# Optimization experiments

Measured on AMD Instinct MI355X. Metric: run time of the kernel, lower is better.

The kernel has to match this reference:

```python
import jax, jax.numpy as jnp
import numpy as np

SCALE = 10.0
KB = 1.0  # kernel_bandwidth

B, D, P, M, K = 128, 128, 4, 100000, 10


def _sqdist(a, b):
    # a: [..., N, D], b: [..., M, D] -> squared euclidean [..., N, M]
    a2 = jnp.sum(a * a, axis=-1)[..., :, None]
    b2 = jnp.sum(b * b, axis=-1)[..., None, :]
    ab = jnp.einsum('...nd,...md->...nm', a, b)
    return jnp.maximum(a2 + b2 - 2.0 * ab, 0.0)


def setup_inputs() -> dict:
    key = jax.random.key(0)
    k1, k2, k3, k4, k5, k6, k7 = jax.random.split(key, 7)
    return {
        'global_img_feat': jax.random.normal(k1, (B, D), jnp.float32),
        'global_text_feat': jax.random.normal(k2, (B, D), jnp.float32),
        'local_img_feats': jax.random.normal(k3, (P, B, D), jnp.float32),
        'centers': jax.random.normal(k4, (P, M, D), jnp.float32),
        'cross_indices': jax.random.randint(k5, (B, K), 0, M, jnp.int64),
        'position': jax.random.randint(k6, (B,), 0, M, jnp.int64),
        'memory_vid': jax.random.randint(k7, (M,), 0, 1000, jnp.int64),
    }


def reference(global_img_feat, global_text_feat, local_img_feats, centers,
              cross_indices, position, memory_vid):
    b = global_img_feat.shape[0]
    # ---- global MMD alignment (text branch detached) ----
    img = global_img_feat / jnp.linalg.norm(global_img_feat, axis=1, keepdims=True)
    txt_d = jax.lax.stop_gradient(global_text_feat)
    txt = txt_d / jnp.linalg.norm(txt_d, axis=1, keepdims=True)
    inv2kb2 = 1.0 / (2.0 * KB * KB)
    k_xx = jnp.exp(-_sqdist(img, img) * inv2kb2)
    k_yy = jnp.exp(-_sqdist(txt, txt) * inv2kb2)
    k_xy = jnp.exp(-_sqdist(img, txt) * inv2kb2)
    off = ~jnp.eye(b, dtype=bool)
    denom = b * (b - 1)
    mmd = (jnp.sum(jnp.where(off, k_xx, 0.0)) / denom
           + jnp.sum(jnp.where(off, k_yy, 0.0)) / denom
           - 2.0 * jnp.mean(k_xy))
    # ---- local part contrastive loss (vectorized over P parts) ----
    m = centers.shape[1]
    pos_feat = centers[:, cross_indices]                       # [P,B,K,D]
    f2 = jnp.sum(local_img_feats ** 2, axis=-1)                # [P,B]
    p2 = jnp.sum(pos_feat ** 2, axis=-1)                       # [P,B,K]
    fp = jnp.einsum('pbd,pbkd->pbk', local_img_feats, pos_feat)
    pos_dist = jnp.sqrt(jnp.maximum(f2[..., None] + p2 - 2.0 * fp, 0.0))  # [P,B,K]
    neg_dist = jnp.sqrt(_sqdist(local_img_feats, centers))     # [P,B,M]
    # negative mask over memory slots (int indices are constants)
    neg_mask = jnp.ones((m,), bool).at[cross_indices.reshape(-1)].set(False)
    neg_mask = neg_mask.at[position].set(False)
    x = jnp.log(jnp.sum(jnp.exp(-SCALE * pos_dist), axis=-1))  # [P,B]
    y = jnp.log(jnp.sum(jnp.exp(-SCALE * neg_dist) * neg_mask[None, None, :], axis=-1))
    l = jnp.sum(-x + y, axis=1) / local_img_feats.shape[1]     # [P]
    l = jnp.where(jnp.isnan(l), 0.0, l)
    local_loss = jnp.sum(l) / local_img_feats.shape[0]
    total = local_loss + 1.0 * mmd
    pos_vid = memory_vid[cross_indices]                        # [B,K]
    return total, local_loss, mmd, pos_vid
```

## Files before the change

kernel.cpp:

```cpp
#include <hip/hip_runtime.h>
#include <math.h>

#define B_ 128
#define D_ 128
#define P_ 4
#define M_ 100000
#define K_ 10
#define SCALE_ 10.0f
#define NEG_BLOCKS 512
#define MMD_BLOCKS 128
#define POS_BLOCKS 128
#define D2_CUT 120.0f

typedef short bf16x8 __attribute__((ext_vector_type(8)));
typedef float floatx4 __attribute__((ext_vector_type(4)));

__device__ inline unsigned pack_bf16_trunc(unsigned f0, unsigned f1) {
    return __builtin_amdgcn_perm(f1, f0, 0x07060302u);
}

template <int CTRL>
__device__ inline float dpp_add(float v) {
    int x = __builtin_amdgcn_update_dpp(0, __builtin_bit_cast(int, v), CTRL, 0xF, 0xF, true);
    return v + __builtin_bit_cast(float, x);
}
__device__ inline float row16Sum(float v) {
    v = dpp_add<0xB1>(v);
    v = dpp_add<0x4E>(v);
    v = dpp_add<0x141>(v);
    v = dpp_add<0x140>(v);
    return v;
}
__device__ inline float waveSum64(float v) {
    v = row16Sum(v);
    v += __shfl_xor(v, 16, 64);
    v += __shfl_xor(v, 32, 64);
    return v;
}
__device__ inline float waveReduceSumOld(float v) {
    #pragma unroll
    for (int off = 32; off > 0; off >>= 1) v += __shfl_xor(v, off, 64);
    return v;
}
__device__ inline float blockReduce128(float v, float* sh2) {
    v = waveSum64(v);
    int wid = threadIdx.x >> 6;
    if ((threadIdx.x & 63) == 0) sh2[wid] = v;
    __syncthreads();
    float r = sh2[0] + sh2[1];
    __syncthreads();
    return r;
}

__global__ __launch_bounds__(128) void k_prep(const float* __restrict__ img,
                                              const float* __restrict__ txt,
                                              const float* __restrict__ local,
                                              float* imgT, float* txtT,
                                              float* a2i, float* a2t,
                                              float* f2w, float* s_neg,
                                              bf16x8* __restrict__ Apk) {
    __shared__ float sh2[2];
    int bid = blockIdx.x, t = threadIdx.x;
    if (bid < 256) {
        int row = bid & 127, which = bid >> 7;
        if (bid < 4) s_neg[bid * 128 + t] = 0.f;
        const float* src = which ? txt : img;
        float* dstT = which ? txtT : imgT;
        float* a2 = which ? a2t : a2i;
        float v = src[row * D_ + t];
        float s = blockReduce128(v * v, sh2);
        float n = v / sqrtf(s);
        dstT[t * 128 + row] = n;
        float s2 = blockReduce128(n * n, sh2);
        if (t == 0) a2[row] = s2;
    } else if (bid < 768) {
        int r = bid - 256;
        float v = local[(size_t)r * D_ + t];
        float s = blockReduce128(v * v, sh2);
        if (t == 0) f2w[r] = s;
    } else {
        int g = (bid - 768) * 128 + t;
        int p = g >> 11, f = g & 2047;
        int fl = f & 63, bt = (f >> 6) & 7, kc = f >> 9;
        int row = bt * 16 + (fl & 15);
        int col = kc * 32 + ((fl >> 4) & 3) * 8;
        const float* lp = local + (size_t)p * B_ * D_ + row * D_ + col;
        const uint4 u0 = *(const uint4*)lp;
        const uint4 u1 = *(const uint4*)(lp + 4);
        union { bf16x8 v; unsigned u[4]; } fr;
        fr.u[0] = pack_bf16_trunc(u0.x, u0.y);
        fr.u[1] = pack_bf16_trunc(u0.z, u0.w);
        fr.u[2] = pack_bf16_trunc(u1.x, u1.y);
        fr.u[3] = pack_bf16_trunc(u1.z, u1.w);
        Apk[g] = fr.v;
    }
}

__global__ __launch_bounds__(256, 2) void k_neg(const float* __restrict__ centers,
                                                const int* __restrict__ ci,
                                                const int* __restrict__ posi,
                                                const float* __restrict__ f2w,
                                                const bf16x8* __restrict__ Apk,
                                                float* __restrict__ s_neg) {
    __shared__ float Bt[2][3][2048];
    const int t = threadIdx.x;
    const int w = t >> 6;
    const int l = t & 63;
    const int bid = blockIdx.x;
    const int p = bid >> 7;
    const int g = bid & 127;
    const int pp = w >> 1;
    const int hm = w & 1;
    const int pairid = 2 * g + pp;
    const int nt = (g < 53) ? 25 : 24;
    const int n16 = l & 15;
    const int q = l >> 4;

    const bf16x8* Ap = Apk + (p << 11);
    bf16x8 af[4][4];
    #pragma unroll
    for (int kc = 0; kc < 4; kc++)
        #pragma unroll
        for (int b4 = 0; b4 < 4; b4++)
            af[kc][b4] = Ap[kc * 512 + (hm * 4 + b4) * 64 + l];
    floatx4 f2r[4];
    #pragma unroll
    for (int b4 = 0; b4 < 4; b4++)
        f2r[b4] = *(const floatx4*)&f2w[p * 128 + (hm * 4 + b4) * 16 + q * 4];

    unsigned srcoff[4];
    #pragma unroll
    for (int j = 0; j < 4; j++) {
        unsigned x = (unsigned)(hm * 4096 + j * 1024 + l * 16);
        unsigned s = (x >> 9) & 7u;
        srcoff[j] = x ^ (s << 4);
    }

    const char* tb0 = (const char*)(centers + (size_t)p * M_ * D_);
    char* myBt = (char*)&Bt[pp][0][0];

    auto DMA = [&](int tl, int buf) {
        const char* src = tb0 + (size_t)tl * 8192;
        char* dst = myBt + buf * 8192 + hm * 4096;
        #pragma unroll
        for (int j = 0; j < 4; j++) {
            __builtin_amdgcn_global_load_lds(
                (const __attribute__((address_space(1))) void*)(src + srcoff[j]),
                (__attribute__((address_space(3))) void*)(dst + j * 1024),
                16, 0, 0);
        }
    };

    float sacc[4][4];
    #pragma unroll
    for (int b4 = 0; b4 < 4; b4++)
        #pragma unroll
        for (int r = 0; r < 4; r++) sacc[b4][r] = 0.f;

    DMA(pairid, 0);
    if (nt > 1) DMA(pairid + 256, 1);
    asm volatile("s_waitcnt vmcnt(4)" ::: "memory");
    __builtin_amdgcn_s_barrier();

    int tli = pairid;
    int ib = 0;
    const unsigned sw = (unsigned)((n16 & 7) << 4);
    for (int i = 0; i < nt; i++) {
        const char* bb = myBt + ib * 8192;
        float c2 = 0.f;
        bf16x8 bfr[4];
        #pragma unroll
        for (int kc = 0; kc < 4; kc++) {
            unsigned t0a = (unsigned)(n16 * 512 + kc * 128 + q * 32);
            union { floatx4 f; uint4 u; } h0, h1;
            h0.f = *(const floatx4*)(bb + (t0a ^ sw));
            h1.f = *(const floatx4*)(bb + ((t0a + 16) ^ sw));
            c2 += h0.f[0]*h0.f[0] + h0.f[1]*h0.f[1] + h0.f[2]*h0.f[2] + h0.f[3]*h0.f[3]
                + h1.f[0]*h1.f[0] + h1.f[1]*h1.f[1] + h1.f[2]*h1.f[2] + h1.f[3]*h1.f[3];
            union { bf16x8 v; unsigned uu[4]; } fr;
            fr.uu[0] = pack_bf16_trunc(h0.u.x, h0.u.y);
            fr.uu[1] = pack_bf16_trunc(h0.u.z, h0.u.w);
            fr.uu[2] = pack_bf16_trunc(h1.u.x, h1.u.y);
            fr.uu[3] = pack_bf16_trunc(h1.u.z, h1.u.w);
            bfr[kc] = fr.v;
        }
        c2 += __shfl_xor(c2, 16, 64);
        c2 += __shfl_xor(c2, 32, 64);
        const float c2v = c2;

        floatx4 acc[4];
        #pragma unroll
        for (int b4 = 0; b4 < 4; b4++) acc[b4] = (floatx4)(0.f);
        #pragma unroll
        for (int kc = 0; kc < 4; kc++) {
            #pragma unroll
            for (int b4 = 0; b4 < 4; b4++)
                acc[b4] = __builtin_amdgcn_mfma_f32_16x16x32_bf16(af[kc][b4], bfr[kc], acc[b4], 0, 0, 0);
        }

        float dmin = 1e30f;
        #pragma unroll
        for (int b4 = 0; b4 < 4; b4++) {
            #pragma unroll
            for (int r = 0; r < 4; r++) {
                float d2 = fmaf(-2.f, acc[b4][r], f2r[b4][r] + c2v);
                dmin = fminf(dmin, d2);
            }
        }
        if (__any(dmin < D2_CUT)) {
            const int gm = tli * 16 + n16;
            float vm = 1.f;
            for (int ii = 0; ii < B_ * K_; ii++) {
                if (ci[ii] == gm) vm = 0.f;
            }
            for (int ii = 0; ii < B_; ii++) {
                if (posi[ii] == gm) vm = 0.f;
            }
            #pragma unroll
            for (int b4 = 0; b4 < 4; b4++) {
                #pragma unroll
                for (int r = 0; r < 4; r++) {
                    float d2 = fmaxf(fmaf(-2.f, acc[b4][r], f2r[b4][r] + c2v), 0.f);
                    if (d2 < D2_CUT) sacc[b4][r] += vm * expf(-SCALE_ * sqrtf(d2));
                }
            }
        }

        if (i + 2 < nt) {
            int b2 = ib + 2; if (b2 >= 3) b2 -= 3;
            DMA(tli + 512, b2);
            asm volatile("s_waitcnt vmcnt(4)" ::: "memory");
        } else if (i + 1 < nt) {
            asm volatile("s_waitcnt vmcnt(0)" ::: "memory");
        }
        __builtin_amdgcn_s_barrier();

        tli += 256;
        ib = (ib + 1 == 3) ? 0 : ib + 1;
    }

    #pragma unroll
    for (int b4 = 0; b4 < 4; b4++) {
        #pragma unroll
        for (int r = 0; r < 4; r++) {
            float s = row16Sum(sacc[b4][r]);
            if (n16 == 0 && s != 0.f)
                atomicAdd(&s_neg[p * 128 + (hm * 4 + b4) * 16 + q * 4 + r], s);
        }
    }
}

__global__ __launch_bounds__(256) void k_mp(const float* __restrict__ local,
                                            const float* __restrict__ centers,
                                            const float* __restrict__ imgT,
                                            const float* __restrict__ txtT,
                                            const float* __restrict__ a2i,
                                            const float* __restrict__ a2t,
                                            const int* __restrict__ ci,
                                            const int* __restrict__ mvid,
                                            const float* __restrict__ f2w,
                                            float* __restrict__ s_pos,
                                            double* __restrict__ mmd_part,
                                            float* __restrict__ out) {
    __shared__ float ri[128], rt[128], sh2[2];
    const int bid = blockIdx.x;
    const int t = threadIdx.x;
    const int w = t >> 6;
    const int l = t & 63;

    if (bid < MMD_BLOCKS) {
        const int i = bid;
        if (t < 128) {
            ri[t] = imgT[t * 128 + i];
            rt[t] = txtT[t * 128 + i];
        }
        __syncthreads();
        float kxx = 0.f, kyy = 0.f, kxy = 0.f;
        if (t < 128) {
            float dxx = 0.f, dyy = 0.f, dxy = 0.f;
            #pragma unroll 4
            for (int d = 0; d < D_; d++) {
                float rid = ri[d], rtd = rt[d];
                float av = imgT[d * 128 + t];
                float bv = txtT[d * 128 + t];
                dxx = fmaf(rid, av, dxx);
                dyy = fmaf(rtd, bv, dyy);
                dxy = fmaf(rid, bv, dxy);
            }
            kxx = (i == t) ? 0.f : expf(-fmaxf(a2i[i] + a2i[t] - 2.f * dxx, 0.f) * 0.5f);
            kyy = (i == t) ? 0.f : expf(-fmaxf(a2t[i] + a2t[t] - 2.f * dyy, 0.f) * 0.5f);
            kxy = expf(-fmaxf(a2i[i] + a2t[t] - 2.f * dxy, 0.f) * 0.5f);
        }
        float sxx = waveReduceSumOld(kxx);
        float syy = waveReduceSumOld(kyy);
        float sxy = waveReduceSumOld(kxy);
        __syncthreads();
        if (t == 0)  { sh2[0] = sxx; }
        if (t == 64) { sh2[1] = sxx; }
        __syncthreads();
        float txx = sh2[0] + sh2[1];
        __syncthreads();
        if (t == 0)  { sh2[0] = syy; }
        if (t == 64) { sh2[1] = syy; }
        __syncthreads();
        float tyy = sh2[0] + sh2[1];
        __syncthreads();
        if (t == 0)  { sh2[0] = sxy; }
        if (t == 64) { sh2[1] = sxy; }
        __syncthreads();
        float txy = sh2[0] + sh2[1];
        if (t == 0) {
            mmd_part[i] = (double)txx;
            mmd_part[128 + i] = (double)tyy;
            mmd_part[256 + i] = (double)txy;
        }
    } else {
        const int pair = (bid - MMD_BLOCKS) * 4 + w;
        const int p = pair >> 7, b = pair & 127;
        const float* f = local + (size_t)pair * D_;
        float f0 = f[l], f1 = f[l + 64];
        float f2v = f2w[pair];
        const float* cb = centers + (size_t)p * M_ * D_;
        float s = 0.f;
        #pragma unroll
        for (int k = 0; k < K_; k++) {
            int idx = ci[b * K_ + k];
            const float* c = cb + (size_t)idx * D_;
            float c0 = c[l], c1 = c[l + 64];
            float p2 = waveSum64(c0 * c0 + c1 * c1);
            float fp = waveSum64(f0 * c0 + f1 * c1);
            float d2 = fmaxf(f2v + p2 - 2.f * fp, 0.f);
            if (d2 < D2_CUT) s += expf(-SCALE_ * sqrtf(d2));
        }
        if (l == 0) s_pos[pair] = s;
        if (p == 0 && l < K_) {
            int ix = ci[b * K_ + l];
            out[3 + b * K_ + l] = (float)mvid[ix];
        }
    }
}

__global__ __launch_bounds__(512) void k_final(const float* __restrict__ s_pos,
                                               const float* __restrict__ s_neg,
                                               const double* __restrict__ mmd_part,
                                               float* out) {
    __shared__ float red[512];
    __shared__ float lp_[4];
    int t = threadIdx.x;
    float x = logf(s_pos[t]);
    float y = logf(s_neg[t]);
    red[t] = -x + y;
    __syncthreads();
    for (int s = 64; s > 0; s >>= 1) {
        if ((t & 127) < s) red[t] += red[t + s];
        __syncthreads();
    }
    if ((t & 127) == 0) {
        float lv = red[t] / (float)B_;
        if (isnan(lv)) lv = 0.f;
        lp_[t >> 7] = lv;
    }
    __syncthreads();
    if (t == 0) {
        float local_loss = (lp_[0] + lp_[1] + lp_[2] + lp_[3]) / (float)P_;
        double sxx = 0.0, syy = 0.0, sxy = 0.0;
        for (int i = 0; i < 128; i++) {
            sxx += mmd_part[i];
            syy += mmd_part[128 + i];
            sxy += mmd_part[256 + i];
        }
        double denom = 128.0 * 127.0;
        float mmd = (float)(sxx / denom + syy / denom - 2.0 * (sxy / (128.0 * 128.0)));
        out[0] = local_loss + mmd;
        out[1] = local_loss;
        out[2] = mmd;
    }
}

extern "C" void kernel_launch(void* const* d_in, const int* in_sizes, int n_in,
                              void* d_out, int out_size, void* d_ws, size_t ws_size,
                              hipStream_t stream) {
    const float* img     = (const float*)d_in[0];
    const float* txt     = (const float*)d_in[1];
    const float* local   = (const float*)d_in[2];
    const float* centers = (const float*)d_in[3];
    const int*   ci      = (const int*)d_in[4];
    const int*   posi    = (const int*)d_in[5];
    const int*   mvid    = (const int*)d_in[6];
    float* out = (float*)d_out;

    char* ws = (char*)d_ws;
    float*  imgT     = (float*)(ws + 0);
    float*  txtT     = (float*)(ws + 65536);
    float*  a2i      = (float*)(ws + 131072);
    float*  a2t      = (float*)(ws + 131584);
    float*  f2w      = (float*)(ws + 132096);
    float*  s_pos    = (float*)(ws + 134144);
    float*  s_neg    = (float*)(ws + 136192);
    double* mmd_part = (double*)(ws + 138240);
    bf16x8* Apk      = (bf16x8*)(ws + 147456);

    k_prep<<<832, 128, 0, stream>>>(img, txt, local, imgT, txtT, a2i, a2t, f2w, s_neg, Apk);
    k_neg<<<NEG_BLOCKS, 256, 0, stream>>>(centers, ci, posi, f2w, Apk, s_neg);
    k_mp<<<MMD_BLOCKS + POS_BLOCKS, 256, 0, stream>>>(
        local, centers, imgT, txtT, a2i, a2t, ci, mvid, f2w, s_pos, mmd_part, out);
    k_final<<<1, 512, 0, stream>>>(s_pos, s_neg, mmd_part, out);
}
```

Measured before the change: 324.2 us.

## Fuse neg and MMD/pos kernels; give each wave full 128-row tiles with private double buffer

Merges the negative-distance kernel and the MMD/positive kernel into one launch, so the small MMD and positive blocks can run alongside the large centers scan instead of after it. Each wave now covers all 128 batch rows against its own 16-center tile, which doubles the A fragments and accumulators held in registers. Each wave also keeps a private LDS double buffer, which removes the block-wide barrier and leaves only per-wave vmcnt waits. The cost is higher register pressure under launch_bounds(256,2), which may cause spills or lower occupancy.

```diff
diff --git a/kernel.cpp b/kernel.cpp
--- a/kernel.cpp
+++ b/kernel.cpp
@@ -96,183 +96,166 @@
     }
 }
 
-__global__ __launch_bounds__(256, 2) void k_neg(const float* __restrict__ centers,
-                                                const int* __restrict__ ci,
-                                                const int* __restrict__ posi,
-                                                const float* __restrict__ f2w,
-                                                const bf16x8* __restrict__ Apk,
-                                                float* __restrict__ s_neg) {
-    __shared__ float Bt[2][3][2048];
-    const int t = threadIdx.x;
-    const int w = t >> 6;
-    const int l = t & 63;
-    const int bid = blockIdx.x;
-    const int p = bid >> 7;
-    const int g = bid & 127;
-    const int pp = w >> 1;
-    const int hm = w & 1;
-    const int pairid = 2 * g + pp;
-    const int nt = (g < 53) ? 25 : 24;
-    const int n16 = l & 15;
-    const int q = l >> 4;
-
-    const bf16x8* Ap = Apk + (p << 11);
-    bf16x8 af[4][4];
-    #pragma unroll
-    for (int kc = 0; kc < 4; kc++)
-        #pragma unroll
-        for (int b4 = 0; b4 < 4; b4++)
-            af[kc][b4] = Ap[kc * 512 + (hm * 4 + b4) * 64 + l];
-    floatx4 f2r[4];
-    #pragma unroll
-    for (int b4 = 0; b4 < 4; b4++)
-        f2r[b4] = *(const floatx4*)&f2w[p * 128 + (hm * 4 + b4) * 16 + q * 4];
-
-    unsigned srcoff[4];
-    #pragma unroll
-    for (int j = 0; j < 4; j++) {
-        unsigned x = (unsigned)(hm * 4096 + j * 1024 + l * 16);
-        unsigned s = (x >> 9) & 7u;
-        srcoff[j] = x ^ (s << 4);
-    }
-
-    const char* tb0 = (const char*)(centers + (size_t)p * M_ * D_);
-    char* myBt = (char*)&Bt[pp][0][0];
-
-    auto DMA = [&](int tl, int buf) {
-        const char* src = tb0 + (size_t)tl * 8192;
-        char* dst = myBt + buf * 8192 + hm * 4096;
-        #pragma unroll
-        for (int j = 0; j < 4; j++) {
-            __builtin_amdgcn_global_load_lds(
-                (const __attribute__((address_space(1))) void*)(src + srcoff[j]),
-                (__attribute__((address_space(3))) void*)(dst + j * 1024),
-                16, 0, 0);
-        }
+__global__ __launch_bounds__(256, 2) void k_negmp(const float* __restrict__ centers,
+                                                  const float* __restrict__ local,
+                                                  const float* __restrict__ imgT,
+                                                  const float* __restrict__ txtT,
+                                                  const float* __restrict__ a2i,
+                                                  const float* __restrict__ a2t,
+                                                  const int* __restrict__ ci,
+                                                  const int* __restrict__ posi,
+                                                  const int* __restrict__ mvid,
+                                                  const float* __restrict__ f2w,
+                                                  const bf16x8* __restrict__ Apk,
+                                                  float* __restrict__ s_neg,
+                                                  float* __restrict__ s_pos,
+                                                  double* __restrict__ mmd_part,
+                                                  float* __restrict__ out) {
+    union Smem {
+        float Bt[4][2][2048];
+        struct { float ri[128], rt[128], sh2[2]; } m;
     };
-
-    float sacc[4][4];
-    #pragma unroll
-    for (int b4 = 0; b4 < 4; b4++)
-        #pragma unroll
-        for (int r = 0; r < 4; r++) sacc[b4][r] = 0.f;
-
-    DMA(pairid, 0);
-    if (nt > 1) DMA(pairid + 256, 1);
-    asm volatile("s_waitcnt vmcnt(4)" ::: "memory");
-    __builtin_amdgcn_s_barrier();
-
-    int tli = pairid;
-    int ib = 0;
-    const unsigned sw = (unsigned)((n16 & 7) << 4);
-    for (int i = 0; i < nt; i++) {
-        const char* bb = myBt + ib * 8192;
-        float c2 = 0.f;
-        bf16x8 bfr[4];
-        #pragma unroll
-        for (int kc = 0; kc < 4; kc++) {
-            unsigned t0a = (unsigned)(n16 * 512 + kc * 128 + q * 32);
-            union { floatx4 f; uint4 u; } h0, h1;
-            h0.f = *(const floatx4*)(bb + (t0a ^ sw));
-            h1.f = *(const floatx4*)(bb + ((t0a + 16) ^ sw));
-            c2 += h0.f[0]*h0.f[0] + h0.f[1]*h0.f[1] + h0.f[2]*h0.f[2] + h0.f[3]*h0.f[3]
-                + h1.f[0]*h1.f[0] + h1.f[1]*h1.f[1] + h1.f[2]*h1.f[2] + h1.f[3]*h1.f[3];
-            union { bf16x8 v; unsigned uu[4]; } fr;
-            fr.uu[0] = pack_bf16_trunc(h0.u.x, h0.u.y);
-            fr.uu[1] = pack_bf16_trunc(h0.u.z, h0.u.w);
-            fr.uu[2] = pack_bf16_trunc(h1.u.x, h1.u.y);
-            fr.uu[3] = pack_bf16_trunc(h1.u.z, h1.u.w);
-            bfr[kc] = fr.v;
-        }
-        c2 += __shfl_xor(c2, 16, 64);
-        c2 += __shfl_xor(c2, 32, 64);
-        const float c2v = c2;
-
-        floatx4 acc[4];
-        #pragma unroll
-        for (int b4 = 0; b4 < 4; b4++) acc[b4] = (floatx4)(0.f);
-        #pragma unroll
-        for (int kc = 0; kc < 4; kc++) {
-            #pragma unroll
-            for (int b4 = 0; b4 < 4; b4++)
-                acc[b4] = __builtin_amdgcn_mfma_f32_16x16x32_bf16(af[kc][b4], bfr[kc], acc[b4], 0, 0, 0);
-        }
-
-        float dmin = 1e30f;
-        #pragma unroll
-        for (int b4 = 0; b4 < 4; b4++) {
-            #pragma unroll
-            for (int r = 0; r < 4; r++) {
-                float d2 = fmaf(-2.f, acc[b4][r], f2r[b4][r] + c2v);
-                dmin = fminf(dmin, d2);
-            }
-        }
-        if (__any(dmin < D2_CUT)) {
-            const int gm = tli * 16 + n16;
-            float vm = 1.f;
-            for (int ii = 0; ii < B_ * K_; ii++) {
-                if (ci[ii] == gm) vm = 0.f;
-            }
-            for (int ii = 0; ii < B_; ii++) {
-                if (posi[ii] == gm) vm = 0.f;
-            }
-            #pragma unroll
-            for (int b4 = 0; b4 < 4; b4++) {
-                #pragma unroll
-                for (int r = 0; r < 4; r++) {
-                    float d2 = fmaxf(fmaf(-2.f, acc[b4][r], f2r[b4][r] + c2v), 0.f);
-                    if (d2 < D2_CUT) sacc[b4][r] += vm * expf(-SCALE_ * sqrtf(d2));
-                }
-            }
-        }
-
-        if (i + 2 < nt) {
-            int b2 = ib + 2; if (b2 >= 3) b2 -= 3;
-            DMA(tli + 512, b2);
-            asm volatile("s_waitcnt vmcnt(4)" ::: "memory");
-        } else if (i + 1 < nt) {
-            asm volatile("s_waitcnt vmcnt(0)" ::: "memory");
-        }
-        __builtin_amdgcn_s_barrier();
-
-        tli += 256;
-        ib = (ib + 1 == 3) ? 0 : ib + 1;
-    }
-
-    #pragma unroll
-    for (int b4 = 0; b4 < 4; b4++) {
-        #pragma unroll
-        for (int r = 0; r < 4; r++) {
-            float s = row16Sum(sacc[b4][r]);
-            if (n16 == 0 && s != 0.f)
-                atomicAdd(&s_neg[p * 128 + (hm * 4 + b4) * 16 + q * 4 + r], s);
-        }
-    }
-}
-
-__global__ __launch_bounds__(256) void k_mp(const float* __restrict__ local,
-                                            const float* __restrict__ centers,
-                                            const float* __restrict__ imgT,
-                                            const float* __restrict__ txtT,
-                                            const float* __restrict__ a2i,
-                                            const float* __restrict__ a2t,
-                                            const int* __restrict__ ci,
-                                            const int* __restrict__ mvid,
-                                            const float* __restrict__ f2w,
-                                            float* __restrict__ s_pos,
-                                            double* __restrict__ mmd_part,
-                                            float* __restrict__ out) {
-    __shared__ float ri[128], rt[128], sh2[2];
+    __shared__ Smem sm;
     const int bid = blockIdx.x;
     const int t = threadIdx.x;
     const int w = t >> 6;
     const int l = t & 63;
 
-    if (bid < MMD_BLOCKS) {
-        const int i = bid;
+    if (bid < NEG_BLOCKS) {
+        const int p = bid >> 7;
+        const int v = ((bid & 127) << 2) + w;
+        const int nt = (v < 106) ? 13 : 12;
+        const int n16 = l & 15;
+        const int q = l >> 4;
+
+        const bf16x8* Ap = Apk + (p << 11);
+        bf16x8 af[4][8];
+        #pragma unroll
+        for (int kc = 0; kc < 4; kc++)
+            #pragma unroll
+            for (int bt = 0; bt < 8; bt++)
+                af[kc][bt] = Ap[kc * 512 + bt * 64 + l];
+        floatx4 f2r[8];
+        #pragma unroll
+        for (int bt = 0; bt < 8; bt++)
+            f2r[bt] = *(const floatx4*)&f2w[p * 128 + bt * 16 + q * 4];
+
+        unsigned srcoff[8];
+        #pragma unroll
+        for (int j = 0; j < 8; j++) {
+            unsigned x = (unsigned)(j * 1024 + l * 16);
+            unsigned s = (x >> 9) & 7u;
+            srcoff[j] = x ^ (s << 4);
+        }
+
+        const char* tb0 = (const char*)(centers + (size_t)p * M_ * D_);
+        char* myBt = (char*)&sm.Bt[w][0][0];
+
+        auto DMA = [&](int tl, int buf) {
+            const char* src = tb0 + (size_t)tl * 8192;
+            char* dst = myBt + buf * 8192;
+            #pragma unroll
+            for (int j = 0; j < 8; j++) {
+                __builtin_amdgcn_global_load_lds(
+                    (const __attribute__((address_space(1))) void*)(src + srcoff[j]),
+                    (__attribute__((address_space(3))) void*)(dst + j * 1024),
+                    16, 0, 0);
+            }
+        };
+
+        float sacc[8][4];
+        #pragma unroll
+        for (int bt = 0; bt < 8; bt++)
+            #pragma unroll
+            for (int r = 0; r < 4; r++) sacc[bt][r] = 0.f;
+
+        DMA(v, 0);
+        DMA(v + 512, 1);
+
+        int tl = v;
+        const unsigned sw = (unsigned)((n16 & 7) << 4);
+        for (int i = 0; i < nt; i++) {
+            if (i + 1 < nt) asm volatile("s_waitcnt vmcnt(8)" ::: "memory");
+            else            asm volatile("s_waitcnt vmcnt(0)" ::: "memory");
+
+            const char* bb = myBt + (i & 1) * 8192;
+            float c2 = 0.f;
+            bf16x8 bfr[4];
+            #pragma unroll
+            for (int kc = 0; kc < 4; kc++) {
+                unsigned t0a = (unsigned)(n16 * 512 + kc * 128 + q * 32);
+                union { floatx4 f; uint4 u; } h0, h1;
+                h0.f = *(const floatx4*)(bb + (t0a ^ sw));
+                h1.f = *(const floatx4*)(bb + ((t0a + 16) ^ sw));
+                c2 += h0.f[0]*h0.f[0] + h0.f[1]*h0.f[1] + h0.f[2]*h0.f[2] + h0.f[3]*h0.f[3]
+                    + h1.f[0]*h1.f[0] + h1.f[1]*h1.f[1] + h1.f[2]*h1.f[2] + h1.f[3]*h1.f[3];
+                union { bf16x8 vv; unsigned uu[4]; } fr;
+                fr.uu[0] = pack_bf16_trunc(h0.u.x, h0.u.y);
+                fr.uu[1] = pack_bf16_trunc(h0.u.z, h0.u.w);
+                fr.uu[2] = pack_bf16_trunc(h1.u.x, h1.u.y);
+                fr.uu[3] = pack_bf16_trunc(h1.u.z, h1.u.w);
+                bfr[kc] = fr.vv;
+            }
+            c2 += __shfl_xor(c2, 16, 64);
+            c2 += __shfl_xor(c2, 32, 64);
+            const float c2v = c2;
+
+            floatx4 acc[8];
+            #pragma unroll
+            for (int bt = 0; bt < 8; bt++) acc[bt] = (floatx4)(0.f);
+            #pragma unroll
+            for (int kc = 0; kc < 4; kc++) {
+                #pragma unroll
+                for (int bt = 0; bt < 8; bt++)
+                    acc[bt] = __builtin_amdgcn_mfma_f32_16x16x32_bf16(af[kc][bt], bfr[kc], acc[bt], 0, 0, 0);
+            }
+
+            float dmin = 1e30f;
+            #pragma unroll
+            for (int bt = 0; bt < 8; bt++) {
+                #pragma unroll
+                for (int r = 0; r < 4; r++) {
+                    float d2 = fmaf(-2.f, acc[bt][r], f2r[bt][r] + c2v);
+                    dmin = fminf(dmin, d2);
+                }
+            }
+            if (__any(dmin < D2_CUT)) {
+                const int gm = tl * 16 + n16;
+                float vm = 1.f;
+                for (int ii = 0; ii < B_ * K_; ii++) {
+                    if (ci[ii] == gm) vm = 0.f;
+                }
+                for (int ii = 0; ii < B_; ii++) {
+                    if (posi[ii] == gm) vm = 0.f;
+                }
+                #pragma unroll
+                for (int bt = 0; bt < 8; bt++) {
+                    #pragma unroll
+                    for (int r = 0; r < 4; r++) {
+                        float d2 = fmaxf(fmaf(-2.f, acc[bt][r], f2r[bt][r] + c2v), 0.f);
+                        if (d2 < D2_CUT) sacc[bt][r] += vm * expf(-SCALE_ * sqrtf(d2));
+                    }
+                }
+            }
+
+            if (i + 2 < nt) DMA(tl + 1024, i & 1);
+            tl += 512;
+        }
+
+        #pragma unroll
+        for (int bt = 0; bt < 8; bt++) {
+            #pragma unroll
+            for (int r = 0; r < 4; r++) {
+                float s = row16Sum(sacc[bt][r]);
+                if (n16 == 0 && s != 0.f)
+                    atomicAdd(&s_neg[p * 128 + bt * 16 + q * 4 + r], s);
+            }
+        }
+    } else if (bid < NEG_BLOCKS + MMD_BLOCKS) {
+        const int i = bid - NEG_BLOCKS;
         if (t < 128) {
-            ri[t] = imgT[t * 128 + i];
-            rt[t] = txtT[t * 128 + i];
+            sm.m.ri[t] = imgT[t * 128 + i];
+            sm.m.rt[t] = txtT[t * 128 + i];
         }
         __syncthreads();
         float kxx = 0.f, kyy = 0.f, kxy = 0.f;
@@ -280,7 +263,7 @@
             float dxx = 0.f, dyy = 0.f, dxy = 0.f;
             #pragma unroll 4
             for (int d = 0; d < D_; d++) {
-                float rid = ri[d], rtd = rt[d];
+                float rid = sm.m.ri[d], rtd = sm.m.rt[d];
                 float av = imgT[d * 128 + t];
                 float bv = txtT[d * 128 + t];
                 dxx = fmaf(rid, av, dxx);
@@ -295,27 +278,27 @@
         float syy = waveReduceSumOld(kyy);
         float sxy = waveReduceSumOld(kxy);
         __syncthreads();
-        if (t == 0)  { sh2[0] = sxx; }
-        if (t == 64) { sh2[1] = sxx; }
-        __syncthreads();
-        float txx = sh2[0] + sh2[1];
-        __syncthreads();
-        if (t == 0)  { sh2[0] = syy; }
-        if (t == 64) { sh2[1] = syy; }
-        __syncthreads();
-        float tyy = sh2[0] + sh2[1];
-        __syncthreads();
-        if (t == 0)  { sh2[0] = sxy; }
-        if (t == 64) { sh2[1] = sxy; }
-        __syncthreads();
-        float txy = sh2[0] + sh2[1];
+        if (t == 0)  { sm.m.sh2[0] = sxx; }
+        if (t == 64) { sm.m.sh2[1] = sxx; }
+        __syncthreads();
+        float txx = sm.m.sh2[0] + sm.m.sh2[1];
+        __syncthreads();
+        if (t == 0)  { sm.m.sh2[0] = syy; }
+        if (t == 64) { sm.m.sh2[1] = syy; }
+        __syncthreads();
+        float tyy = sm.m.sh2[0] + sm.m.sh2[1];
+        __syncthreads();
+        if (t == 0)  { sm.m.sh2[0] = sxy; }
+        if (t == 64) { sm.m.sh2[1] = sxy; }
+        __syncthreads();
+        float txy = sm.m.sh2[0] + sm.m.sh2[1];
         if (t == 0) {
             mmd_part[i] = (double)txx;
             mmd_part[128 + i] = (double)tyy;
             mmd_part[256 + i] = (double)txy;
         }
     } else {
-        const int pair = (bid - MMD_BLOCKS) * 4 + w;
+        const int pair = (bid - (NEG_BLOCKS + MMD_BLOCKS)) * 4 + w;
         const int p = pair >> 7, b = pair & 127;
         const float* f = local + (size_t)pair * D_;
         float f0 = f[l], f1 = f[l + 64];
@@ -401,8 +384,8 @@
     bf16x8* Apk      = (bf16x8*)(ws + 147456);
 
     k_prep<<<832, 128, 0, stream>>>(img, txt, local, imgT, txtT, a2i, a2t, f2w, s_neg, Apk);
-    k_neg<<<NEG_BLOCKS, 256, 0, stream>>>(centers, ci, posi, f2w, Apk, s_neg);
-    k_mp<<<MMD_BLOCKS + POS_BLOCKS, 256, 0, stream>>>(
-        local, centers, imgT, txtT, a2i, a2t, ci, mvid, f2w, s_pos, mmd_part, out);
+    k_negmp<<<NEG_BLOCKS + MMD_BLOCKS + POS_BLOCKS, 256, 0, stream>>>(
+        centers, local, imgT, txtT, a2i, a2t, ci, posi, mvid, f2w, Apk,
+        s_neg, s_pos, mmd_part, out);
     k_final<<<1, 512, 0, stream>>>(s_pos, s_neg, mmd_part, out);
 }
```

After: 337.1 us. 4.0% more time.

## Stage center tiles through registers into a double-buffered LDS instead of direct DMA

Applied to the files above, without the earlier changes.

The negative-distance kernel no longer uses global_load_lds direct-to-LDS copies into a triple buffer. Each thread now loads the next center tile into registers one iteration ahead, alternating between two register sets. It writes that tile into a two-slot LDS buffer at the end of each iteration, then waits on LDS counters and a barrier. This cuts shared memory per block and may let more blocks run per CU. In exchange it uses more registers and adds explicit LDS store instructions to every iteration.

```diff
diff --git a/kernel.cpp b/kernel.cpp
--- a/kernel.cpp
+++ b/kernel.cpp
@@ -102,7 +102,7 @@
                                                 const float* __restrict__ f2w,
                                                 const bf16x8* __restrict__ Apk,
                                                 float* __restrict__ s_neg) {
-    __shared__ float Bt[2][3][2048];
+    __shared__ float Bt[2][2][2048];
     const int t = threadIdx.x;
     const int w = t >> 6;
     const int l = t & 63;
@@ -138,18 +138,29 @@
 
     const char* tb0 = (const char*)(centers + (size_t)p * M_ * D_);
     char* myBt = (char*)&Bt[pp][0][0];
-
-    auto DMA = [&](int tl, int buf) {
+    char* wdst = myBt + hm * 4096 + l * 16;
+
+    uint4 sA[4], sB[4];
+    auto LOADT_A = [&](int tl) {
         const char* src = tb0 + (size_t)tl * 8192;
-        char* dst = myBt + buf * 8192 + hm * 4096;
-        #pragma unroll
-        for (int j = 0; j < 4; j++) {
-            __builtin_amdgcn_global_load_lds(
-                (const __attribute__((address_space(1))) void*)(src + srcoff[j]),
-                (__attribute__((address_space(3))) void*)(dst + j * 1024),
-                16, 0, 0);
-        }
+        #pragma unroll
+        for (int j = 0; j < 4; j++) sA[j] = *(const uint4*)(src + srcoff[j]);
     };
+    auto LOADT_B = [&](int tl) {
+        const char* src = tb0 + (size_t)tl * 8192;
+        #pragma unroll
+        for (int j = 0; j < 4; j++) sB[j] = *(const uint4*)(src + srcoff[j]);
+    };
+    auto DSW_A = [&](int buf) {
+        char* dst = wdst + buf * 8192;
+        #pragma unroll
+        for (int j = 0; j < 4; j++) *(uint4*)(dst + j * 1024) = sA[j];
+    };
+    auto DSW_B = [&](int buf) {
+        char* dst = wdst + buf * 8192;
+        #pragma unroll
+        for (int j = 0; j < 4; j++) *(uint4*)(dst + j * 1024) = sB[j];
+    };
 
     float sacc[4][4];
     #pragma unroll
@@ -157,16 +168,16 @@
         #pragma unroll
         for (int r = 0; r < 4; r++) sacc[b4][r] = 0.f;
 
-    DMA(pairid, 0);
-    if (nt > 1) DMA(pairid + 256, 1);
-    asm volatile("s_waitcnt vmcnt(4)" ::: "memory");
+    LOADT_A(pairid);
+    LOADT_B(pairid + 256);
+    DSW_A(0);
+    asm volatile("s_waitcnt lgkmcnt(0)" ::: "memory");
     __builtin_amdgcn_s_barrier();
 
     int tli = pairid;
-    int ib = 0;
     const unsigned sw = (unsigned)((n16 & 7) << 4);
     for (int i = 0; i < nt; i++) {
-        const char* bb = myBt + ib * 8192;
+        const char* bb = myBt + (i & 1) * 8192;
         float c2 = 0.f;
         bf16x8 bfr[4];
         #pragma unroll
@@ -227,16 +238,17 @@
         }
 
         if (i + 2 < nt) {
-            int b2 = ib + 2; if (b2 >= 3) b2 -= 3;
-            DMA(tli + 512, b2);
-            asm volatile("s_waitcnt vmcnt(4)" ::: "memory");
-        } else if (i + 1 < nt) {
-            asm volatile("s_waitcnt vmcnt(0)" ::: "memory");
-        }
+            if (i & 1) LOADT_B(tli + 512);
+            else       LOADT_A(tli + 512);
+        }
+        if (i + 1 < nt) {
+            if (i & 1) DSW_A((i + 1) & 1);
+            else       DSW_B((i + 1) & 1);
+        }
+        asm volatile("s_waitcnt lgkmcnt(0)" ::: "memory");
         __builtin_amdgcn_s_barrier();
 
         tli += 256;
-        ib = (ib + 1 == 3) ? 0 : ib + 1;
     }
 
     #pragma unroll
```

Measured after the change: 344.7 us. +6.3%, slower.

## Fuse negative-distance and MMD/positive kernels; assign contiguous tile ranges per wave pair

Applied to the files above, without the earlier changes.

Merges the k_neg and k_mp kernels into one launch. The MMD and positive-pair blocks become extra blocks after the 512 negative-scan blocks, and the two shared-memory layouts are overlaid in a union. Each wave pair also now walks a contiguous run of 25 or 24 center tiles instead of tiles strided by 256, which changes the DRAM access pattern. The aim is to remove one launch and its tail gap, and to let the small MMD and positive blocks run alongside the bandwidth-bound scan. In exchange, the shared union forces the small blocks to reserve the large LDS footprint, and the fused kernel may use more registers.

```diff
diff --git a/kernel.cpp b/kernel.cpp
--- a/kernel.cpp
+++ b/kernel.cpp
@@ -96,183 +96,177 @@
     }
 }
 
-__global__ __launch_bounds__(256, 2) void k_neg(const float* __restrict__ centers,
-                                                const int* __restrict__ ci,
-                                                const int* __restrict__ posi,
-                                                const float* __restrict__ f2w,
-                                                const bf16x8* __restrict__ Apk,
-                                                float* __restrict__ s_neg) {
-    __shared__ float Bt[2][3][2048];
+__global__ __launch_bounds__(256, 2) void k_negmp(const float* __restrict__ centers,
+                                                  const float* __restrict__ local,
+                                                  const float* __restrict__ imgT,
+                                                  const float* __restrict__ txtT,
+                                                  const float* __restrict__ a2i,
+                                                  const float* __restrict__ a2t,
+                                                  const int* __restrict__ ci,
+                                                  const int* __restrict__ posi,
+                                                  const int* __restrict__ mvid,
+                                                  const float* __restrict__ f2w,
+                                                  const bf16x8* __restrict__ Apk,
+                                                  float* __restrict__ s_neg,
+                                                  float* __restrict__ s_pos,
+                                                  double* __restrict__ mmd_part,
+                                                  float* __restrict__ out) {
+    union Smem {
+        struct { float Bt[2][3][2048]; } n;
+        struct { float ri[128], rt[128], sh2[2]; } m;
+    };
+    __shared__ Smem sm;
     const int t = threadIdx.x;
     const int w = t >> 6;
     const int l = t & 63;
     const int bid = blockIdx.x;
-    const int p = bid >> 7;
-    const int g = bid & 127;
-    const int pp = w >> 1;
-    const int hm = w & 1;
-    const int pairid = 2 * g + pp;
-    const int nt = (g < 53) ? 25 : 24;
-    const int n16 = l & 15;
-    const int q = l >> 4;
-
-    const bf16x8* Ap = Apk + (p << 11);
-    bf16x8 af[4][4];
-    #pragma unroll
-    for (int kc = 0; kc < 4; kc++)
+
+    if (bid < NEG_BLOCKS) {
+        const int p = bid >> 7;
+        const int g = bid & 127;
+        const int pp = w >> 1;
+        const int hm = w & 1;
+        const int pairid = 2 * g + pp;
+        const int nt = (g < 53) ? 25 : 24;
+        const int base = (pairid < 106) ? pairid * 25 : 2650 + (pairid - 106) * 24;
+        const int n16 = l & 15;
+        const int q = l >> 4;
+
+        const bf16x8* Ap = Apk + (p << 11);
+        bf16x8 af[4][4];
+        #pragma unroll
+        for (int kc = 0; kc < 4; kc++)
+            #pragma unroll
+            for (int b4 = 0; b4 < 4; b4++)
+                af[kc][b4] = Ap[kc * 512 + (hm * 4 + b4) * 64 + l];
+        floatx4 f2r[4];
         #pragma unroll
         for (int b4 = 0; b4 < 4; b4++)
-            af[kc][b4] = Ap[kc * 512 + (hm * 4 + b4) * 64 + l];
-    floatx4 f2r[4];
-    #pragma unroll
-    for (int b4 = 0; b4 < 4; b4++)
-        f2r[b4] = *(const floatx4*)&f2w[p * 128 + (hm * 4 + b4) * 16 + q * 4];
-
-    unsigned srcoff[4];
-    #pragma unroll
-    for (int j = 0; j < 4; j++) {
-        unsigned x = (unsigned)(hm * 4096 + j * 1024 + l * 16);
-        unsigned s = (x >> 9) & 7u;
-        srcoff[j] = x ^ (s << 4);
-    }
-
-    const char* tb0 = (const char*)(centers + (size_t)p * M_ * D_);
-    char* myBt = (char*)&Bt[pp][0][0];
-
-    auto DMA = [&](int tl, int buf) {
-        const char* src = tb0 + (size_t)tl * 8192;
-        char* dst = myBt + buf * 8192 + hm * 4096;
+            f2r[b4] = *(const floatx4*)&f2w[p * 128 + (hm * 4 + b4) * 16 + q * 4];
+
+        unsigned srcoff[4];
         #pragma unroll
         for (int j = 0; j < 4; j++) {
-            __builtin_amdgcn_global_load_lds(
-                (const __attribute__((address_space(1))) void*)(src + srcoff[j]),
-                (__attribute__((address_space(3))) void*)(dst + j * 1024),
-                16, 0, 0);
-        }
-    };
-
-    float sacc[4][4];
-    #pragma unroll
-    for (int b4 = 0; b4 < 4; b4++)
-        #pragma unroll
-        for (int r = 0; r < 4; r++) sacc[b4][r] = 0.f;
-
-    DMA(pairid, 0);
-    if (nt > 1) DMA(pairid + 256, 1);
-    asm volatile("s_waitcnt vmcnt(4)" ::: "memory");
-    __builtin_amdgcn_s_barrier();
-
-    int tli = pairid;
-    int ib = 0;
-    const unsigned sw = (unsigned)((n16 & 7) << 4);
-    for (int i = 0; i < nt; i++) {
-        const char* bb = myBt + ib * 8192;
-        float c2 = 0.f;
-        bf16x8 bfr[4];
-        #pragma unroll
-        for (int kc = 0; kc < 4; kc++) {
-            unsigned t0a = (unsigned)(n16 * 512 + kc * 128 + q * 32);
-            union { floatx4 f; uint4 u; } h0, h1;
-            h0.f = *(const floatx4*)(bb + (t0a ^ sw));
-            h1.f = *(const floatx4*)(bb + ((t0a + 16) ^ sw));
-            c2 += h0.f[0]*h0.f[0] + h0.f[1]*h0.f[1] + h0.f[2]*h0.f[2] + h0.f[3]*h0.f[3]
-                + h1.f[0]*h1.f[0] + h1.f[1]*h1.f[1] + h1.f[2]*h1.f[2] + h1.f[3]*h1.f[3];
-            union { bf16x8 v; unsigned uu[4]; } fr;
-            fr.uu[0] = pack_bf16_trunc(h0.u.x, h0.u.y);
-            fr.uu[1] = pack_bf16_trunc(h0.u.z, h0.u.w);
-            fr.uu[2] = pack_bf16_trunc(h1.u.x, h1.u.y);
-            fr.uu[3] = pack_bf16_trunc(h1.u.z, h1.u.w);
-            bfr[kc] = fr.v;
-        }
-        c2 += __shfl_xor(c2, 16, 64);
-        c2 += __shfl_xor(c2, 32, 64);
-        const float c2v = c2;
-
-        floatx4 acc[4];
-        #pragma unroll
-        for (int b4 = 0; b4 < 4; b4++) acc[b4] = (floatx4)(0.f);
-        #pragma unroll
-        for (int kc = 0; kc < 4; kc++) {
-            #pragma unroll
-            for (int b4 = 0; b4 < 4; b4++)
-                acc[b4] = __builtin_amdgcn_mfma_f32_16x16x32_bf16(af[kc][b4], bfr[kc], acc[b4], 0, 0, 0);
-        }
-
-        float dmin = 1e30f;
-        #pragma unroll
-        for (int b4 = 0; b4 < 4; b4++) {
-            #pragma unroll
-            for (int r = 0; r < 4; r++) {
-                float d2 = fmaf(-2.f, acc[b4][r], f2r[b4][r] + c2v);
-                dmin = fminf(dmin, d2);
-            }
-        }
-        if (__any(dmin < D2_CUT)) {
-            const int gm = tli * 16 + n16;
-            float vm = 1.f;
-            for (int ii = 0; ii < B_ * K_; ii++) {
-                if (ci[ii] == gm) vm = 0.f;
-            }
-            for (int ii = 0; ii < B_; ii++) {
-                if (posi[ii] == gm) vm = 0.f;
-            }
+            unsigned x = (unsigned)(hm * 4096 + j * 1024 + l * 16);
+            unsigned s = (x >> 9) & 7u;
+            srcoff[j] = x ^ (s << 4);
+        }
+
+        const char* tb0 = (const char*)(centers + (size_t)p * M_ * D_);
+        char* myBt = (char*)&sm.n.Bt[pp][0][0];
+
+        auto DMA = [&](int tl, int buf) {
+            const char* src = tb0 + (size_t)tl * 8192;
+            char* dst = myBt + buf * 8192 + hm * 4096;
+            #pragma unroll
+            for (int j = 0; j < 4; j++) {
+                __builtin_amdgcn_global_load_lds(
+                    (const __attribute__((address_space(1))) void*)(src + srcoff[j]),
+                    (__attribute__((address_space(3))) void*)(dst + j * 1024),
+                    16, 0, 0);
+            }
+        };
+
+        float sacc[4][4];
+        #pragma unroll
+        for (int b4 = 0; b4 < 4; b4++)
+            #pragma unroll
+            for (int r = 0; r < 4; r++) sacc[b4][r] = 0.f;
+
+        DMA(base, 0);
+        DMA(base + 1, 1);
+        asm volatile("s_waitcnt vmcnt(4)" ::: "memory");
+        __builtin_amdgcn_s_barrier();
+
+        int ib = 0;
+        const unsigned sw = (unsigned)((n16 & 7) << 4);
+        for (int i = 0; i < nt; i++) {
+            const char* bb = myBt + ib * 8192;
+            float c2 = 0.f;
+            bf16x8 bfr[4];
+            #pragma unroll
+            for (int kc = 0; kc < 4; kc++) {
+                unsigned t0a = (unsigned)(n16 * 512 + kc * 128 + q * 32);
+                union { floatx4 f; uint4 u; } h0, h1;
+                h0.f = *(const floatx4*)(bb + (t0a ^ sw));
+                h1.f = *(const floatx4*)(bb + ((t0a + 16) ^ sw));
+                c2 += h0.f[0]*h0.f[0] + h0.f[1]*h0.f[1] + h0.f[2]*h0.f[2] + h0.f[3]*h0.f[3]
+                    + h1.f[0]*h1.f[0] + h1.f[1]*h1.f[1] + h1.f[2]*h1.f[2] + h1.f[3]*h1.f[3];
+                union { bf16x8 v; unsigned uu[4]; } fr;
+                fr.uu[0] = pack_bf16_trunc(h0.u.x, h0.u.y);
+                fr.uu[1] = pack_bf16_trunc(h0.u.z, h0.u.w);
+                fr.uu[2] = pack_bf16_trunc(h1.u.x, h1.u.y);
+                fr.uu[3] = pack_bf16_trunc(h1.u.z, h1.u.w);
+                bfr[kc] = fr.v;
+            }
+            c2 += __shfl_xor(c2, 16, 64);
+            c2 += __shfl_xor(c2, 32, 64);
+            const float c2v = c2;
+
+            floatx4 acc[4];
+            #pragma unroll
+            for (int b4 = 0; b4 < 4; b4++) acc[b4] = (floatx4)(0.f);
+            #pragma unroll
+            for (int kc = 0; kc < 4; kc++) {
+                #pragma unroll
+                for (int b4 = 0; b4 < 4; b4++)
+                    acc[b4] = __builtin_amdgcn_mfma_f32_16x16x32_bf16(af[kc][b4], bfr[kc], acc[b4], 0, 0, 0);
+            }
+
+            float dmin = 1e30f;
             #pragma unroll
             for (int b4 = 0; b4 < 4; b4++) {
                 #pragma unroll
                 for (int r = 0; r < 4; r++) {
-                    float d2 = fmaxf(fmaf(-2.f, acc[b4][r], f2r[b4][r] + c2v), 0.f);
-                    if (d2 < D2_CUT) sacc[b4][r] += vm * expf(-SCALE_ * sqrtf(d2));
+                    float d2 = fmaf(-2.f, acc[b4][r], f2r[b4][r] + c2v);
+                    dmin = fminf(dmin, d2);
                 }
             }
-        }
-
-        if (i + 2 < nt) {
-            int b2 = ib + 2; if (b2 >= 3) b2 -= 3;
-            DMA(tli + 512, b2);
-            asm volatile("s_waitcnt vmcnt(4)" ::: "memory");
-        } else if (i + 1 < nt) {
-            asm volatile("s_waitcnt vmcnt(0)" ::: "memory");
-        }
-        __builtin_amdgcn_s_barrier();
-
-        tli += 256;
-        ib = (ib + 1 == 3) ? 0 : ib + 1;
-    }
-
-    #pragma unroll
-    for (int b4 = 0; b4 < 4; b4++) {
-        #pragma unroll
-        for (int r = 0; r < 4; r++) {
-            float s = row16Sum(sacc[b4][r]);
-            if (n16 == 0 && s != 0.f)
-                atomicAdd(&s_neg[p * 128 + (hm * 4 + b4) * 16 + q * 4 + r], s);
-        }
-    }
-}
-
-__global__ __launch_bounds__(256) void k_mp(const float* __restrict__ local,
-                                            const float* __restrict__ centers,
-                                            const float* __restrict__ imgT,
-                                            const float* __restrict__ txtT,
-                                            const float* __restrict__ a2i,
-                                            const float* __restrict__ a2t,
-                                            const int* __restrict__ ci,
-                                            const int* __restrict__ mvid,
-                                            const float* __restrict__ f2w,
-                                            float* __restrict__ s_pos,
-                                            double* __restrict__ mmd_part,
-                                            float* __restrict__ out) {
-    __shared__ float ri[128], rt[128], sh2[2];
-    const int bid = blockIdx.x;
-    const int t = threadIdx.x;
-    const int w = t >> 6;
-    const int l = t & 63;
-
-    if (bid < MMD_BLOCKS) {
-        const int i = bid;
+            if (__any(dmin < D2_CUT)) {
+                const int gm = (base + i) * 16 + n16;
+                float vm = 1.f;
+                for (int ii = 0; ii < B_ * K_; ii++) {
+                    if (ci[ii] == gm) vm = 0.f;
+                }
+                for (int ii = 0; ii < B_; ii++) {
+                    if (posi[ii] == gm) vm = 0.f;
+                }
+                #pragma unroll
+                for (int b4 = 0; b4 < 4; b4++) {
+                    #pragma unroll
+                    for (int r = 0; r < 4; r++) {
+                        float d2 = fmaxf(fmaf(-2.f, acc[b4][r], f2r[b4][r] + c2v), 0.f);
+                        if (d2 < D2_CUT) sacc[b4][r] += vm * expf(-SCALE_ * sqrtf(d2));
+                    }
+                }
+            }
+
+            if (i + 2 < nt) {
+                int b2 = ib + 2; if (b2 >= 3) b2 -= 3;
+                DMA(base + i + 2, b2);
+                asm volatile("s_waitcnt vmcnt(4)" ::: "memory");
+            } else if (i + 1 < nt) {
+                asm volatile("s_waitcnt vmcnt(0)" ::: "memory");
+            }
+            __builtin_amdgcn_s_barrier();
+
+            ib = (ib + 1 == 3) ? 0 : ib + 1;
+        }
+
+        #pragma unroll
+        for (int b4 = 0; b4 < 4; b4++) {
+            #pragma unroll
+            for (int r = 0; r < 4; r++) {
+                float s = row16Sum(sacc[b4][r]);
+                if (n16 == 0 && s != 0.f)
+                    atomicAdd(&s_neg[p * 128 + (hm * 4 + b4) * 16 + q * 4 + r], s);
+            }
+        }
+    } else if (bid < NEG_BLOCKS + MMD_BLOCKS) {
+        const int i = bid - NEG_BLOCKS;
         if (t < 128) {
-            ri[t] = imgT[t * 128 + i];
-            rt[t] = txtT[t * 128 + i];
+            sm.m.ri[t] = imgT[t * 128 + i];
+            sm.m.rt[t] = txtT[t * 128 + i];
         }
         __syncthreads();
         float kxx = 0.f, kyy = 0.f, kxy = 0.f;
@@ -280,7 +274,7 @@
             float dxx = 0.f, dyy = 0.f, dxy = 0.f;
             #pragma unroll 4
             for (int d = 0; d < D_; d++) {
-                float rid = ri[d], rtd = rt[d];
+                float rid = sm.m.ri[d], rtd = sm.m.rt[d];
                 float av = imgT[d * 128 + t];
                 float bv = txtT[d * 128 + t];
                 dxx = fmaf(rid, av, dxx);
@@ -295,27 +289,27 @@
         float syy = waveReduceSumOld(kyy);
         float sxy = waveReduceSumOld(kxy);
         __syncthreads();
-        if (t == 0)  { sh2[0] = sxx; }
-        if (t == 64) { sh2[1] = sxx; }
-        __syncthreads();
-        float txx = sh2[0] + sh2[1];
-        __syncthreads();
-        if (t == 0)  { sh2[0] = syy; }
-        if (t == 64) { sh2[1] = syy; }
-        __syncthreads();
-        float tyy = sh2[0] + sh2[1];
-        __syncthreads();
-        if (t == 0)  { sh2[0] = sxy; }
-        if (t == 64) { sh2[1] = sxy; }
-        __syncthreads();
-        float txy = sh2[0] + sh2[1];
+        if (t == 0)  { sm.m.sh2[0] = sxx; }
+        if (t == 64) { sm.m.sh2[1] = sxx; }
+        __syncthreads();
+        float txx = sm.m.sh2[0] + sm.m.sh2[1];
+        __syncthreads();
+        if (t == 0)  { sm.m.sh2[0] = syy; }
+        if (t == 64) { sm.m.sh2[1] = syy; }
+        __syncthreads();
+        float tyy = sm.m.sh2[0] + sm.m.sh2[1];
+        __syncthreads();
+        if (t == 0)  { sm.m.sh2[0] = sxy; }
+        if (t == 64) { sm.m.sh2[1] = sxy; }
+        __syncthreads();
+        float txy = sm.m.sh2[0] + sm.m.sh2[1];
         if (t == 0) {
             mmd_part[i] = (double)txx;
             mmd_part[128 + i] = (double)tyy;
             mmd_part[256 + i] = (double)txy;
         }
     } else {
-        const int pair = (bid - MMD_BLOCKS) * 4 + w;
+        const int pair = (bid - (NEG_BLOCKS + MMD_BLOCKS)) * 4 + w;
         const int p = pair >> 7, b = pair & 127;
         const float* f = local + (size_t)pair * D_;
         float f0 = f[l], f1 = f[l + 64];
@@ -401,8 +395,8 @@
     bf16x8* Apk      = (bf16x8*)(ws + 147456);
 
     k_prep<<<832, 128, 0, stream>>>(img, txt, local, imgT, txtT, a2i, a2t, f2w, s_neg, Apk);
-    k_neg<<<NEG_BLOCKS, 256, 0, stream>>>(centers, ci, posi, f2w, Apk, s_neg);
-    k_mp<<<MMD_BLOCKS + POS_BLOCKS, 256, 0, stream>>>(
-        local, centers, imgT, txtT, a2i, a2t, ci, mvid, f2w, s_pos, mmd_part, out);
+    k_negmp<<<NEG_BLOCKS + MMD_BLOCKS + POS_BLOCKS, 256, 0, stream>>>(
+        centers, local, imgT, txtT, a2i, a2t, ci, posi, mvid, f2w, Apk,
+        s_neg, s_pos, mmd_part, out);
     k_final<<<1, 512, 0, stream>>>(s_pos, s_neg, mmd_part, out);
 }
```

Result: no change. 318.6 us (-1.7%).
